# Performance work log

Hardware: AMD Instinct MI355X
Metric: run time of the kernel (lower is better)

## Reference

```python
import math
import jax, jax.numpy as jnp
import numpy as np

K = 1.0            # Lorentz manifold curvature k
B, S = 4, 2048     # batch, seq_len
IN, H, OUT = 512, 8, 64   # in_channels, num_heads, out_channels (space dim; head_dim = OUT+1)


def setup_inputs() -> dict:
    key = jax.random.key(0)
    ks = jax.random.split(key, 8)
    std = 1.0 / math.sqrt(IN)
    return {
        "query_input": jax.random.normal(ks[0], (B, S, IN), jnp.float32),
        "source_input": jax.random.normal(ks[1], (B, S, IN), jnp.float32),
        # per-head HypLinear weights stacked on a leading head axis: [H, OUT, IN]
        "Wq_w": jax.random.normal(ks[2], (H, OUT, IN), jnp.float32) * std,
        "Wq_b": jnp.zeros((H, OUT), jnp.float32),
        "Wk_w": jax.random.normal(ks[3], (H, OUT, IN), jnp.float32) * std,
        "Wk_b": jnp.zeros((H, OUT), jnp.float32),
        "Wv_w": jax.random.normal(ks[4], (H, OUT, IN), jnp.float32) * std,
        "Wv_b": jnp.zeros((H, OUT), jnp.float32),
        "scale": jnp.array([math.sqrt(OUT)], jnp.float32),  # nn.Parameter([sqrt(out_channels)])
        "bias": jnp.zeros((), jnp.float32),                 # nn.Parameter(zeros(()))
    }


def hyp_linear(x, w, b):
    # HypLinear: linear map to space part, recompute Lorentz time coord sqrt(||x_s||^2 + k)
    sp = jnp.einsum('bsi,hoi->bsho', x, w) + b            # [B,S,H,OUT]
    t = jnp.sqrt(jnp.sum(sp * sp, axis=-1, keepdims=True) + K)
    return jnp.concatenate([t, sp], axis=-1)              # [B,S,H,OUT+1]


def reference(query_input, source_input, Wq_w, Wq_b, Wk_w, Wk_b, Wv_w, Wv_b, scale, bias):
    q = hyp_linear(query_input, Wq_w, Wq_b)   # [B,S,H,D], D = OUT+1
    k = hyp_linear(source_input, Wk_w, Wk_b)
    v = hyp_linear(source_input, Wv_w, Wv_b)

    # Lorentzian cinner: <x,y>_L = -x0*y0 + <x_s, y_s>
    sgn = jnp.concatenate([-jnp.ones((1,), q.dtype), jnp.ones((OUT,), q.dtype)])
    att = jnp.einsum('bqhd,bkhd->bhqk', q * sgn, k)       # [B,H,S,S]
    att = (2.0 + 2.0 * att) / scale[0] + bias

    causal = jnp.triu(jnp.full((S, S), -1e9, q.dtype), 1)  # causal mask (additive)
    att = jax.nn.softmax(att + causal, axis=-1)

    ctx = jnp.einsum('bhqk,bkhd->bqhd', att, v)           # [B,S,H,D]

    # manifold.mid_point over the heads axis (dim=-2)
    ave = jnp.mean(ctx, axis=2)                           # [B,S,D]
    inner = -ave[..., :1] ** 2 + jnp.sum(ave[..., 1:] ** 2, axis=-1, keepdims=True)
    denom = jnp.sqrt(jnp.maximum(jnp.abs(-inner), 1e-8))
    return math.sqrt(K) * ave / denom                     # [B,S,D]
```

## Files before the change

kernel.cpp:

```cpp
#include <hip/hip_runtime.h>

#define BATCH 4
#define SEQ   2048
#define INC   512
#define NH    8
#define OUTC  64
#define DD    65
#define NROW  (BATCH * NH * SEQ)
#define PSTRIDE 72

typedef float f32x4 __attribute__((ext_vector_type(4)));
typedef short short8 __attribute__((ext_vector_type(8)));
typedef short short4v __attribute__((ext_vector_type(4)));
typedef unsigned int uint2v __attribute__((ext_vector_type(2)));
typedef unsigned short us;

static __device__ __forceinline__ us f2b(float f) {
  unsigned int u = __float_as_uint(f);
  u = (u + 0x7FFFu + ((u >> 16) & 1u)) >> 16;
  return (us)u;
}
static __device__ __forceinline__ float b2f(us h) {
  return __uint_as_float(((unsigned int)h) << 16);
}
static __device__ __forceinline__ unsigned int pk2(float lo, float hi) {
  unsigned int r;
  asm("v_cvt_pk_bf16_f32 %0, %1, %2" : "=v"(r) : "v"(lo), "v"(hi));
  return r;
}

#define GLDS(g, l) __builtin_amdgcn_global_load_lds( \
    (const __attribute__((address_space(1))) void*)(g), \
    (__attribute__((address_space(3))) void*)(l), 16, 0, 0)
#define SB() __builtin_amdgcn_sched_barrier(0)

__global__ __launch_bounds__(256) void tobf16_kernel(
    const float* __restrict__ Xq, const float* __restrict__ Xs,
    const float* __restrict__ Wq, const float* __restrict__ Wk,
    const float* __restrict__ Wv,
    us* __restrict__ dXq, us* __restrict__ dXs,
    us* __restrict__ dWq, us* __restrict__ dWk, us* __restrict__ dWv)
{
  const int which = blockIdx.y;
  const float* src;
  us* dst;
  int n;
  switch (which) {
    case 0: src = Xq; dst = dXq; n = BATCH * SEQ * INC; break;
    case 1: src = Xs; dst = dXs; n = BATCH * SEQ * INC; break;
    case 2: src = Wq; dst = dWq; n = NH * OUTC * INC; break;
    case 3: src = Wk; dst = dWk; n = NH * OUTC * INC; break;
    default: src = Wv; dst = dWv; n = NH * OUTC * INC; break;
  }
  for (long i = (long)blockIdx.x * 256 + threadIdx.x; i * 4 < n;
       i += (long)gridDim.x * 256) {
    f32x4 v = *(const f32x4*)(src + i * 4);
    short4v o;
    o[0] = (short)f2b(v[0]); o[1] = (short)f2b(v[1]);
    o[2] = (short)f2b(v[2]); o[3] = (short)f2b(v[3]);
    *(short4v*)(dst + i * 4) = o;
  }
}

__global__ __launch_bounds__(256) void proj_kernel(
    const us* __restrict__ Xqb, const us* __restrict__ Xsb,
    const us* __restrict__ Wqb, const us* __restrict__ Wkb, const us* __restrict__ Wvb,
    const float* __restrict__ Bq, const float* __restrict__ Bk, const float* __restrict__ Bv,
    const float* __restrict__ scale_p,
    us* __restrict__ qs, unsigned int* __restrict__ qta,
    us* __restrict__ ks, unsigned int* __restrict__ kta,
    us* __restrict__ vT, us* __restrict__ vtc)
{
  const int which = blockIdx.z;
  const us* X = (which == 0) ? Xqb : Xsb;
  const us* W = (which == 0) ? Wqb : (which == 1 ? Wkb : Wvb);
  const float* Bb = (which == 0) ? Bq : (which == 1 ? Bk : Bv);
  const float al2 = (2.0f / scale_p[0]) * 1.44269504088896f;
  const float oscale = (which == 0) ? al2 : 1.0f;

  const int lin = blockIdx.x;
  const int h   = (lin >> 3) & 7;
  const int m0  = (((lin >> 6) << 3) | (lin & 7)) * 64;
  const int n0  = h * 64;

  __shared__ alignas(16) us lXf[2 * 64 * 64];
  __shared__ alignas(16) us lWf[2 * 64 * 64];

  const int tid  = threadIdx.x;
  const int lane = tid & 63;
  const int wave = tid >> 6;
  const int arow = lane & 15;
  const int agrp = lane >> 4;
  const int rl   = lane >> 3;
  const int chx  = ((lane & 7) ^ rl) * 8;
  const int r0   = wave * 8 + rl;
  const int r1   = r0 + 32;

#define PSTAGE(buf, k0) do { \
    GLDS(X + (size_t)(m0 + r0) * INC + (k0) + chx, &lXf[(buf) * 4096 + wave * 512]); \
    GLDS(X + (size_t)(m0 + r1) * INC + (k0) + chx, &lXf[(buf) * 4096 + 2048 + wave * 512]); \
    GLDS(W + (size_t)(n0 + r0) * INC + (k0) + chx, &lWf[(buf) * 4096 + wave * 512]); \
    GLDS(W + (size_t)(n0 + r1) * INC + (k0) + chx, &lWf[(buf) * 4096 + 2048 + wave * 512]); \
  } while (0)

  f32x4 acc[4] = {};
  PSTAGE(0, 0);

  for (int kk = 0; kk < 8; ++kk) {
    const int cur = kk & 1;
    if (kk < 7) {
      PSTAGE(cur ^ 1, (kk + 1) * 64);
      asm volatile("s_waitcnt vmcnt(4)");
    } else {
      asm volatile("s_waitcnt vmcnt(0)");
    }
    __builtin_amdgcn_s_barrier();
#pragma unroll
    for (int kc = 0; kc < 2; ++kc) {
      short8 af = *(const short8*)&lXf[cur * 4096 + (wave * 16 + arow) * 64 + (((kc * 4 + agrp) ^ (arow & 7)) * 8)];
#pragma unroll
      for (int c = 0; c < 4; ++c) {
        short8 bf = *(const short8*)&lWf[cur * 4096 + (c * 16 + arow) * 64 + (((kc * 4 + agrp) ^ (arow & 7)) * 8)];
        acc[c] = __builtin_amdgcn_mfma_f32_16x16x32_bf16(af, bf, acc[c], 0, 0, 0);
      }
    }
    __builtin_amdgcn_s_barrier();
  }

  float bcol[4];
#pragma unroll
  for (int c = 0; c < 4; ++c) bcol[c] = Bb[n0 + c * 16 + arow];

  us* lT = &lXf[0];

#pragma unroll
  for (int r = 0; r < 4; ++r) {
    float s2 = 0.f;
#pragma unroll
    for (int c = 0; c < 4; ++c) {
      float v = acc[c][r] + bcol[c];
      acc[c][r] = v;
      s2 += v * v;
    }
    s2 += __shfl_xor(s2, 1); s2 += __shfl_xor(s2, 2);
    s2 += __shfl_xor(s2, 4); s2 += __shfl_xor(s2, 8);
    float tv = sqrtf(s2 + 1.0f);
    int gs = m0 + wave * 16 + agrp * 4 + r;
    int bi = gs >> 11, si = gs & (SEQ - 1);
    size_t rowbase = (size_t)(bi * NH + h) * SEQ + si;
    if (which == 2) {
      int lrow = wave * 16 + agrp * 4 + r;
#pragma unroll
      for (int c = 0; c < 4; ++c)
        lT[lrow * PSTRIDE + c * 16 + arow] = f2b(acc[c][r]);
      if (arow == 0) {
        us th = f2b(tv);
        us tl = f2b(tv - b2f(th));
        vtc[rowbase] = th;
        vtc[NROW + rowbase] = tl;
      }
    } else {
      us* outs = (which == 0) ? qs : ks;
      size_t obase = rowbase * 64;
#pragma unroll
      for (int c = 0; c < 4; ++c) outs[obase + c * 16 + arow] = f2b(oscale * acc[c][r]);
      if (arow == 0) {
        if (which == 0) {
          float st = al2 * tv;
          us qh = f2b(st);
          us ql = f2b(st - b2f(qh));
          qta[rowbase] = (unsigned int)qh | ((unsigned int)ql << 16);
        } else {
          kta[rowbase] = (unsigned int)(us)(f2b(tv) ^ 0x8000)
                       | ((unsigned int)(us)(f2b(tv - b2f(f2b(tv))) ^ 0x8000) << 16);
        }
      }
    }
  }

  if (which == 2) {
    __syncthreads();
    const int bi = m0 >> 11, si0 = m0 & (SEQ - 1);
    us* vbase = vT + ((size_t)(bi * NH + h) * 64) * SEQ + si0;
#pragma unroll
    for (int u0 = 0; u0 < 2; ++u0) {
      int u = tid + u0 * 256;
      int o = u >> 3, jc = u & 7;
      short8 w;
#pragma unroll
      for (int j = 0; j < 8; ++j) w[j] = (short)lT[(jc * 8 + j) * PSTRIDE + o];
      *(short8*)(vbase + (size_t)o * SEQ + jc * 8) = w;
    }
  }
}

__global__ __launch_bounds__(512) void attn_kernel(
    const us* __restrict__ qs, const unsigned int* __restrict__ qta,
    const us* __restrict__ ks, const unsigned int* __restrict__ kta,
    const us* __restrict__ vT, const us* __restrict__ vtc,
    us* __restrict__ part)
{
  const int f = blockIdx.x;
  const int xcd = f & 7, idx = f >> 3;
  const int bh = xcd * 4 + (idx / 24);
  const int inner = idx % 24;
  const int x = inner / 3;
  const int s = inner % 3;
  const int n0 = 2 * x + 2;
  const int n1 = 32 - 2 * x;

  __shared__ alignas(16) us lK[2][64 * 64];
  __shared__ alignas(16) us lV[2][64 * 64];
  __shared__ alignas(16) us lP[8][16 * 40];

  const int tid  = threadIdx.x;
  const int lane = tid & 63;
  const int wave = tid >> 6;
  const int arow = lane & 15;
  const int agrp = lane >> 4;

  const size_t bhbase = (size_t)bh * SEQ;
  const us* kgp = ks + bhbase * 64;
  const us* vgp = vT + (size_t)bh * 64 * SEQ;
  const unsigned int* ktp = kta + bhbase;
  const us* vtp = vtc + (size_t)(arow & 1) * NROW + bhbase;

  const int rl   = lane >> 3;
  const int chx  = ((lane & 7) ^ rl) * 8;
  const int dsl0 = (agrp ^ (arow & 7)) * 8;
  const int dsl1 = ((4 + agrp) ^ (arow & 7)) * 8;
  us* myP = &lP[wave][0];
  const int pw0 = arow * 40 + agrp * 4;
  const int prd = arow * 40 + agrp * 8;

#define ASTAGE(buf, t64) do { \
    const int kk = (t64) * 64; \
    GLDS(kgp + (size_t)(kk + wave * 8 + rl) * 64 + chx, &lK[buf][wave * 512]); \
    GLDS(vgp + (size_t)(wave * 8 + rl) * SEQ + kk + chx, &lV[buf][wave * 512]); \
  } while (0)

  short8 ones8, zero8 = {};
#pragma unroll
  for (int j = 0; j < 8; ++j) ones8[j] = (short)0x3F80;

  for (int seg = 0; seg < 2; ++seg) {
    const int qT = seg ? (15 - x) : x;
    int lo, hi;
    if (seg == 0) { lo = min(12 * s, n0);          hi = min(12 * s + 12, n0); }
    else          { lo = max(12 * s - n0, 0);      hi = min(12 * s + 12 - n0, n1); }
    const int nt = hi - lo;
    if (nt <= 0) continue;

    const int wq = qT * 128 + wave * 16 + arow;
    f32x4 acc[5] = {};

    const us* qp = qs + (bhbase + wq) * 64;
    short8 qf0 = *(const short8*)(qp + agrp * 8);
    short8 qf1 = *(const short8*)(qp + 32 + agrp * 8);
    unsigned int qw = qta[bhbase + wq];
    short8 qf2 = {};
    if (agrp == 0) {
      qf2[0] = (short)(qw & 0xFFFFu);
      qf2[1] = (short)(qw & 0xFFFFu);
      qf2[2] = (short)(qw >> 16);
    }

    unsigned int ka[4];
    short8 va0, va1;
    {
      const int kk = lo * 64;
#pragma unroll
      for (int c = 0; c < 4; ++c) ka[c] = ktp[kk + c * 16 + arow];
      va0 = *(const short8*)(vtp + kk + agrp * 8);
      va1 = *(const short8*)(vtp + kk + 32 + agrp * 8);
    }
    SB();
    ASTAGE(0, lo);
    SB();

    for (int it = 0; it < nt; ++it) {
      const int t = lo + it;
      const int cur = it & 1;
      if (it < nt - 1) {
        ASTAGE(cur ^ 1, t + 1);
        SB();
        asm volatile("s_waitcnt vmcnt(2)");
      } else {
        SB();
        asm volatile("s_waitcnt vmcnt(0)");
      }
      SB();
      __builtin_amdgcn_s_barrier();

      const us* Kb = lK[cur];
      const us* Vb = lV[cur];

      f32x4 sS[4] = {};
      __builtin_amdgcn_s_setprio(1);
#pragma unroll
      for (int c = 0; c < 4; ++c) {
        short8 kf = *(const short8*)&Kb[(c * 16 + arow) * 64 + dsl0];
        sS[c] = __builtin_amdgcn_mfma_f32_16x16x32_bf16(kf, qf0, sS[c], 0, 0, 0);
      }
#pragma unroll
      for (int c = 0; c < 4; ++c) {
        short8 kf = *(const short8*)&Kb[(c * 16 + arow) * 64 + dsl1];
        sS[c] = __builtin_amdgcn_mfma_f32_16x16x32_bf16(kf, qf1, sS[c], 0, 0, 0);
      }
#pragma unroll
      for (int c = 0; c < 4; ++c) {
        short8 kf2 = {};
        if (agrp == 0) {
          unsigned int w0 = ka[c];
          kf2[0] = (short)(w0 & 0xFFFFu);
          kf2[1] = (short)(w0 >> 16);
          kf2[2] = (short)(w0 & 0xFFFFu);
        }
        sS[c] = __builtin_amdgcn_mfma_f32_16x16x32_bf16(kf2, qf2, sS[c], 0, 0, 0);
      }
      __builtin_amdgcn_s_setprio(0);

#pragma unroll
      for (int c = 0; c < 4; ++c)
#pragma unroll
        for (int r = 0; r < 4; ++r)
          sS[c][r] = exp2f(sS[c][r]);
      if (t >= 2 * qT) {
        const int kb = t * 64;
#pragma unroll
        for (int c = 0; c < 4; ++c)
#pragma unroll
          for (int r = 0; r < 4; ++r)
            if (kb + c * 16 + agrp * 4 + r > wq) sS[c][r] = 0.f;
      }

      {
        uint2v w;
        w[0] = pk2(sS[0][0], sS[0][1]); w[1] = pk2(sS[0][2], sS[0][3]);
        *(uint2v*)&myP[pw0] = w;
        w[0] = pk2(sS[1][0], sS[1][1]); w[1] = pk2(sS[1][2], sS[1][3]);
        *(uint2v*)&myP[pw0 + 16] = w;
        short8 pf = *(const short8*)&myP[prd];
        __builtin_amdgcn_s_setprio(1);
#pragma unroll
        for (int dc = 0; dc < 4; ++dc) {
          short8 vf = *(const short8*)&Vb[(dc * 16 + arow) * 64 + dsl0];
          acc[dc] = __builtin_amdgcn_mfma_f32_16x16x32_bf16(pf, vf, acc[dc], 0, 0, 0);
        }
        short8 vf4 = (arow < 2) ? va0 : ((arow == 2) ? ones8 : zero8);
        acc[4] = __builtin_amdgcn_mfma_f32_16x16x32_bf16(pf, vf4, acc[4], 0, 0, 0);
        __builtin_amdgcn_s_setprio(0);
      }
      {
        uint2v w;
        w[0] = pk2(sS[2][0], sS[2][1]); w[1] = pk2(sS[2][2], sS[2][3]);
        *(uint2v*)&myP[pw0] = w;
        w[0] = pk2(sS[3][0], sS[3][1]); w[1] = pk2(sS[3][2], sS[3][3]);
        *(uint2v*)&myP[pw0 + 16] = w;
        short8 pf = *(const short8*)&myP[prd];
        __builtin_amdgcn_s_setprio(1);
#pragma unroll
        for (int dc = 0; dc < 4; ++dc) {
          short8 vf = *(const short8*)&Vb[(dc * 16 + arow) * 64 + dsl1];
          acc[dc] = __builtin_amdgcn_mfma_f32_16x16x32_bf16(pf, vf, acc[dc], 0, 0, 0);
        }
        short8 vf4 = (arow < 2) ? va1 : ((arow == 2) ? ones8 : zero8);
        acc[4] = __builtin_amdgcn_mfma_f32_16x16x32_bf16(pf, vf4, acc[4], 0, 0, 0);
        __builtin_amdgcn_s_setprio(0);
      }

      SB();
      if (it + 1 < nt) {
        const int kk = (t + 1) * 64;
#pragma unroll
        for (int c = 0; c < 4; ++c) ka[c] = ktp[kk + c * 16 + arow];
        va0 = *(const short8*)(vtp + kk + agrp * 8);
        va1 = *(const short8*)(vtp + kk + 32 + agrp * 8);
      }
      SB();
      __builtin_amdgcn_s_barrier();
    }

    const size_t pb = ((size_t)(bh * 16 + qT) * 3 + s) * 128;
#pragma unroll
    for (int r = 0; r < 4; ++r) {
      float t0 = __shfl(acc[4][r], (agrp << 4) | 0);
      float t1 = __shfl(acc[4][r], (agrp << 4) | 1);
      float ls = __shfl(acc[4][r], (agrp << 4) | 2);
      size_t rp = (pb + wave * 16 + agrp * 4 + r) * PSTRIDE;
#pragma unroll
      for (int dc = 0; dc < 4; ++dc)
        part[rp + dc * 16 + arow] = f2b(acc[dc][r]);
      if (arow == 0) {
        float* fp = (float*)(part + rp + 64);
        fp[0] = t0 + t1;
        fp[1] = ls;
      }
    }
  }
}

__global__ __launch_bounds__(256) void finalize_kernel(
    const us* __restrict__ part, float* __restrict__ out)
{
  const int tid  = threadIdx.x;
  const int lane = tid & 63;
  const int gw = blockIdx.x * 4 + (tid >> 6);
  const int b = gw >> 11, si = gw & (SEQ - 1);
  const int qT = si >> 7, row = si & 127;

  const bool v0 = (qT <= 7) || (qT >= 11);
  const bool v1 = (qT >= 6);
  const bool v2 = (qT >= 8);

  float vsum = 0.f, tsum = 0.f;
#pragma unroll
  for (int h = 0; h < NH; ++h) {
    const size_t tb = ((size_t)(b * NH + h) * 16 + qT) * 3;
    float Ah = 0.f, Th = 0.f, Lh = 0.f;
    if (v0) {
      size_t rb = ((tb + 0) * 128 + row) * PSTRIDE;
      Ah += b2f(part[rb + lane]);
      const float* fp = (const float*)(part + rb + 64);
      Th += fp[0]; Lh += fp[1];
    }
    if (v1) {
      size_t rb = ((tb + 1) * 128 + row) * PSTRIDE;
      Ah += b2f(part[rb + lane]);
      const float* fp = (const float*)(part + rb + 64);
      Th += fp[0]; Lh += fp[1];
    }
    if (v2) {
      size_t rb = ((tb + 2) * 128 + row) * PSTRIDE;
      Ah += b2f(part[rb + lane]);
      const float* fp = (const float*)(part + rb + 64);
      Th += fp[0]; Lh += fp[1];
    }
    float inv = 1.0f / Lh;
    vsum = fmaf(Ah, inv, vsum);
    tsum = fmaf(Th, inv, tsum);
  }
  float ave  = vsum * 0.125f;
  float tave = tsum * 0.125f;
  float contrib = ave * ave;
  if (lane == 0) contrib -= tave * tave;
  contrib += __shfl_xor(contrib, 1);
  contrib += __shfl_xor(contrib, 2);
  contrib += __shfl_xor(contrib, 4);
  contrib += __shfl_xor(contrib, 8);
  contrib += __shfl_xor(contrib, 16);
  contrib += __shfl_xor(contrib, 32);
  float denom = sqrtf(fmaxf(fabsf(contrib), 1e-8f));
  size_t ob = ((size_t)b * SEQ + si) * (size_t)DD;
  out[ob + 1 + lane] = ave / denom;
  if (lane == 0) out[ob] = tave / denom;
}

extern "C" void kernel_launch(void* const* d_in, const int* in_sizes, int n_in,
                              void* d_out, int out_size, void* d_ws, size_t ws_size,
                              hipStream_t stream) {
  const float* Xq  = (const float*)d_in[0];
  const float* Xs  = (const float*)d_in[1];
  const float* Wq  = (const float*)d_in[2];
  const float* Bq  = (const float*)d_in[3];
  const float* Wk  = (const float*)d_in[4];
  const float* Bk  = (const float*)d_in[5];
  const float* Wv  = (const float*)d_in[6];
  const float* Bv  = (const float*)d_in[7];
  const float* scale = (const float*)d_in[8];
  float* out = (float*)d_out;

  char* p = (char*)d_ws;

  us* partw = (us*)p;
  us* Xqb   = (us*)p;
  us* Xsb   = (us*)(p + 16777216);
  us* Wqb16 = (us*)(p + 33554432);
  us* Wkb16 = (us*)(p + 34078720);
  us* Wvb16 = (us*)(p + 34603008);
  p += 35651584;
  us* qsb = (us*)p; p += (size_t)NROW * 64 * 2;
  us* ksb = (us*)p; p += (size_t)NROW * 64 * 2;
  us* vTb = (us*)p; p += (size_t)NROW * 64 * 2;
  unsigned int* qtaw = (unsigned int*)p; p += (size_t)NROW * 4;
  unsigned int* ktaw = (unsigned int*)p; p += (size_t)NROW * 4;
  us* vtcw = (us*)p; p += (size_t)NROW * 2 * 2;

  tobf16_kernel<<<dim3(1024, 5), 256, 0, stream>>>(
      Xq, Xs, Wq, Wk, Wv, Xqb, Xsb, Wqb16, Wkb16, Wvb16);
  proj_kernel<<<dim3(1024, 1, 3), 256, 0, stream>>>(
      Xqb, Xsb, Wqb16, Wkb16, Wvb16, Bq, Bk, Bv, scale,
      qsb, qtaw, ksb, ktaw, vTb, vtcw);
  attn_kernel<<<dim3(768), 512, 0, stream>>>(
      qsb, qtaw, ksb, ktaw, vTb, vtcw, partw);
  finalize_kernel<<<(BATCH * SEQ) / 4, 256, 0, stream>>>(partw, out);
}
```

Measured before the change: 96.30 us.

## Fuse fp32-to-bf16 activation conversion into projection kernel loads

The projection kernel now reads fp32 activations straight into registers, converts them to bf16, and writes them into swizzled LDS. The separate pass that converted X to bf16 (a write then re-read of 32 MB) is removed, and only the weights are still pre-converted. In exchange each projection block reads twice the activation bytes from global memory (fp32 instead of bf16). The same activations are read once per head block, so this extra traffic is repeated, and the pipeline now waits on vmcnt(0) with an extra conversion step in every k-iteration.

```diff
diff --git a/kernel.cpp b/kernel.cpp
--- a/kernel.cpp
+++ b/kernel.cpp
@@ -28,6 +28,12 @@
   asm("v_cvt_pk_bf16_f32 %0, %1, %2" : "=v"(r) : "v"(lo), "v"(hi));
   return r;
 }
+static __device__ __forceinline__ short8 mk8(unsigned int a, unsigned int b,
+                                             unsigned int c, unsigned int d) {
+  union { unsigned int u[4]; short8 s; } x;
+  x.u[0] = a; x.u[1] = b; x.u[2] = c; x.u[3] = d;
+  return x.s;
+}
 
 #define GLDS(g, l) __builtin_amdgcn_global_load_lds( \
     (const __attribute__((address_space(1))) void*)(g), \
@@ -35,23 +41,14 @@
 #define SB() __builtin_amdgcn_sched_barrier(0)
 
 __global__ __launch_bounds__(256) void tobf16_kernel(
-    const float* __restrict__ Xq, const float* __restrict__ Xs,
     const float* __restrict__ Wq, const float* __restrict__ Wk,
     const float* __restrict__ Wv,
-    us* __restrict__ dXq, us* __restrict__ dXs,
     us* __restrict__ dWq, us* __restrict__ dWk, us* __restrict__ dWv)
 {
   const int which = blockIdx.y;
-  const float* src;
-  us* dst;
-  int n;
-  switch (which) {
-    case 0: src = Xq; dst = dXq; n = BATCH * SEQ * INC; break;
-    case 1: src = Xs; dst = dXs; n = BATCH * SEQ * INC; break;
-    case 2: src = Wq; dst = dWq; n = NH * OUTC * INC; break;
-    case 3: src = Wk; dst = dWk; n = NH * OUTC * INC; break;
-    default: src = Wv; dst = dWv; n = NH * OUTC * INC; break;
-  }
+  const float* src = (which == 0) ? Wq : (which == 1 ? Wk : Wv);
+  us* dst = (which == 0) ? dWq : (which == 1 ? dWk : dWv);
+  const int n = NH * OUTC * INC;
   for (long i = (long)blockIdx.x * 256 + threadIdx.x; i * 4 < n;
        i += (long)gridDim.x * 256) {
     f32x4 v = *(const f32x4*)(src + i * 4);
@@ -63,7 +60,7 @@
 }
 
 __global__ __launch_bounds__(256) void proj_kernel(
-    const us* __restrict__ Xqb, const us* __restrict__ Xsb,
+    const float* __restrict__ Xq, const float* __restrict__ Xs,
     const us* __restrict__ Wqb, const us* __restrict__ Wkb, const us* __restrict__ Wvb,
     const float* __restrict__ Bq, const float* __restrict__ Bk, const float* __restrict__ Bv,
     const float* __restrict__ scale_p,
@@ -72,7 +69,7 @@
     us* __restrict__ vT, us* __restrict__ vtc)
 {
   const int which = blockIdx.z;
-  const us* X = (which == 0) ? Xqb : Xsb;
+  const float* Xf = (which == 0) ? Xq : Xs;
   const us* W = (which == 0) ? Wqb : (which == 1 ? Wkb : Wvb);
   const float* Bb = (which == 0) ? Bq : (which == 1 ? Bk : Bv);
   const float al2 = (2.0f / scale_p[0]) * 1.44269504088896f;
@@ -95,26 +92,48 @@
   const int chx  = ((lane & 7) ^ rl) * 8;
   const int r0   = wave * 8 + rl;
   const int r1   = r0 + 32;
-
-#define PSTAGE(buf, k0) do { \
-    GLDS(X + (size_t)(m0 + r0) * INC + (k0) + chx, &lXf[(buf) * 4096 + wave * 512]); \
-    GLDS(X + (size_t)(m0 + r1) * INC + (k0) + chx, &lXf[(buf) * 4096 + 2048 + wave * 512]); \
+  const int xrow  = tid >> 3;
+  const int xch   = tid & 7;
+  const int xslot = xch ^ (xrow & 7);
+
+#define WSTAGE(buf, k0) do { \
     GLDS(W + (size_t)(n0 + r0) * INC + (k0) + chx, &lWf[(buf) * 4096 + wave * 512]); \
     GLDS(W + (size_t)(n0 + r1) * INC + (k0) + chx, &lWf[(buf) * 4096 + 2048 + wave * 512]); \
   } while (0)
 
+  f32x4 xa0, xb0, xa1, xb1;
+#define XLOAD(k0) do { \
+    const float* xb = Xf + (size_t)(m0 + xrow) * INC + (k0) + xch * 8; \
+    xa0 = *(const f32x4*)xb;              xb0 = *(const f32x4*)(xb + 4); \
+    xa1 = *(const f32x4*)(xb + 32 * INC); xb1 = *(const f32x4*)(xb + 32 * INC + 4); \
+  } while (0)
+#define XWRITE(buf) do { \
+    *(short8*)&lXf[(buf) * 4096 + xrow * 64 + xslot * 8] = \
+        mk8(pk2(xa0[0], xa0[1]), pk2(xa0[2], xa0[3]), \
+            pk2(xb0[0], xb0[1]), pk2(xb0[2], xb0[3])); \
+    *(short8*)&lXf[(buf) * 4096 + 2048 + xrow * 64 + xslot * 8] = \
+        mk8(pk2(xa1[0], xa1[1]), pk2(xa1[2], xa1[3]), \
+            pk2(xb1[0], xb1[1]), pk2(xb1[2], xb1[3])); \
+  } while (0)
+
   f32x4 acc[4] = {};
-  PSTAGE(0, 0);
+
+  XLOAD(0);
+  WSTAGE(0, 0);
+  SB();
+  asm volatile("s_waitcnt vmcnt(0)");
+  XWRITE(0);
+  asm volatile("s_waitcnt lgkmcnt(0)");
+  SB();
+  __builtin_amdgcn_s_barrier();
 
   for (int kk = 0; kk < 8; ++kk) {
     const int cur = kk & 1;
     if (kk < 7) {
-      PSTAGE(cur ^ 1, (kk + 1) * 64);
-      asm volatile("s_waitcnt vmcnt(4)");
-    } else {
-      asm volatile("s_waitcnt vmcnt(0)");
-    }
-    __builtin_amdgcn_s_barrier();
+      WSTAGE(cur ^ 1, (kk + 1) * 64);
+      XLOAD((kk + 1) * 64);
+    }
+    SB();
 #pragma unroll
     for (int kc = 0; kc < 2; ++kc) {
       short8 af = *(const short8*)&lXf[cur * 4096 + (wave * 16 + arow) * 64 + (((kc * 4 + agrp) ^ (arow & 7)) * 8)];
@@ -124,8 +143,16 @@
         acc[c] = __builtin_amdgcn_mfma_f32_16x16x32_bf16(af, bf, acc[c], 0, 0, 0);
       }
     }
-    __builtin_amdgcn_s_barrier();
+    SB();
+    if (kk < 7) {
+      asm volatile("s_waitcnt vmcnt(0)");
+      XWRITE(cur ^ 1);
+      asm volatile("s_waitcnt lgkmcnt(0)");
+      SB();
+      __builtin_amdgcn_s_barrier();
+    }
   }
+  __syncthreads();
 
   float bcol[4];
 #pragma unroll
@@ -473,12 +500,10 @@
   char* p = (char*)d_ws;
 
   us* partw = (us*)p;
-  us* Xqb   = (us*)p;
-  us* Xsb   = (us*)(p + 16777216);
-  us* Wqb16 = (us*)(p + 33554432);
-  us* Wkb16 = (us*)(p + 34078720);
-  us* Wvb16 = (us*)(p + 34603008);
-  p += 35651584;
+  us* Wqb16 = (us*)(p + 28311552);
+  us* Wkb16 = (us*)(p + 28835840);
+  us* Wvb16 = (us*)(p + 29360128);
+  p += 29884416;
   us* qsb = (us*)p; p += (size_t)NROW * 64 * 2;
   us* ksb = (us*)p; p += (size_t)NROW * 64 * 2;
   us* vTb = (us*)p; p += (size_t)NROW * 64 * 2;
@@ -486,10 +511,10 @@
   unsigned int* ktaw = (unsigned int*)p; p += (size_t)NROW * 4;
   us* vtcw = (us*)p; p += (size_t)NROW * 2 * 2;
 
-  tobf16_kernel<<<dim3(1024, 5), 256, 0, stream>>>(
-      Xq, Xs, Wq, Wk, Wv, Xqb, Xsb, Wqb16, Wkb16, Wvb16);
+  tobf16_kernel<<<dim3(256, 3), 256, 0, stream>>>(
+      Wq, Wk, Wv, Wqb16, Wkb16, Wvb16);
   proj_kernel<<<dim3(1024, 1, 3), 256, 0, stream>>>(
-      Xqb, Xsb, Wqb16, Wkb16, Wvb16, Bq, Bk, Bv, scale,
+      Xq, Xs, Wqb16, Wkb16, Wvb16, Bq, Bk, Bv, scale,
       qsb, qtaw, ksb, ktaw, vTb, vtcw);
   attn_kernel<<<dim3(768), 512, 0, stream>>>(
       qsb, qtaw, ksb, ktaw, vTb, vtcw, partw);
```

Measured after the change: 99.38 us. 3.2% more time.
